# Kernel tuning notes

Measured on AMD Instinct MI355X. Metric: run time of the kernel, lower is better.

Reference implementation:

```python
import jax, jax.numpy as jnp
import numpy as np

B, T, QL, KVL, D, H = 4, 512, 2, 1, 1024, 16
N = T * QL          # query tokens for self-attn
HD = D // H
MLP_H = 4 * D
EPS_ADA = 1e-6
EPS_LN = 1e-5
NEG = -10000.0


def _ln(x, eps):
    mu = jnp.mean(x, axis=-1, keepdims=True)
    xc = x - mu
    var = jnp.mean(xc * xc, axis=-1, keepdims=True)
    return xc * jax.lax.rsqrt(var + eps)


def _attention(xq, xk, xv, wq, wk, wv, wo, bo, mask, pad_add):
    # xq:[B,Nq,D] xk/xv:[B,Nk,D]; mask:[Nq,Nk] bool; pad_add:[B,1,1,Nk]
    qh = (xq @ wq).reshape(B, -1, H, HD).transpose(0, 2, 1, 3)
    kh = (xk @ wk).reshape(B, -1, H, HD).transpose(0, 2, 1, 3)
    vh = (xv @ wv).reshape(B, -1, H, HD).transpose(0, 2, 1, 3)
    dots = jnp.einsum('bhnd,bhmd->bhnm', qh, kh) * (HD ** -0.5)
    dots = jnp.where(mask[None, None], dots, jnp.asarray(NEG, dots.dtype))
    dots = dots + pad_add
    attn = jax.nn.softmax(dots, axis=-1)
    out = jnp.einsum('bhnm,bhmd->bhnd', attn, vh)
    out = out.transpose(0, 2, 1, 3).reshape(B, -1, D)
    return out @ wo + bo


def setup_inputs() -> dict:
    key = jax.random.key(0)
    ks = jax.random.split(key, 32)
    s = 0.02
    d = {
        'q': jax.random.normal(ks[0], (B, N, D), jnp.float32),
        'c': jax.random.normal(ks[1], (B, T, D), jnp.float32),
        'pe': jax.random.normal(ks[2], (B, T, D), jnp.float32),
        'padding_mask': jax.random.randint(ks[3], (B, T), 0, 2, jnp.int32),
        'w_mod': jax.random.normal(ks[4], (D, 6 * D), jnp.float32) * s,
        'b_mod': jnp.zeros((6 * D,), jnp.float32),
        'sa_wq': jax.random.normal(ks[5], (D, D), jnp.float32) * s,
        'sa_wk': jax.random.normal(ks[6], (D, D), jnp.float32) * s,
        'sa_wv': jax.random.normal(ks[7], (D, D), jnp.float32) * s,
        'sa_wo': jax.random.normal(ks[8], (D, D), jnp.float32) * s,
        'sa_bo': jnp.zeros((D,), jnp.float32),
        'ca_wq': jax.random.normal(ks[9], (D, D), jnp.float32) * s,
        'ca_wk': jax.random.normal(ks[10], (D, D), jnp.float32) * s,
        'ca_wv': jax.random.normal(ks[11], (D, D), jnp.float32) * s,
        'ca_wo': jax.random.normal(ks[12], (D, D), jnp.float32) * s,
        'ca_bo': jnp.zeros((D,), jnp.float32),
        'gk': jnp.ones((D,), jnp.float32), 'bk': jnp.zeros((D,), jnp.float32),
        'gv': jnp.ones((D,), jnp.float32), 'bv': jnp.zeros((D,), jnp.float32),
        'w_alpha': jax.random.normal(ks[13], (2 * D, D), jnp.float32) * s,
        'b_alpha': jnp.zeros((D,), jnp.float32),
        'w1': jax.random.normal(ks[14], (D, MLP_H), jnp.float32) * s,
        'b1': jnp.zeros((MLP_H,), jnp.float32),
        'w2': jax.random.normal(ks[15], (MLP_H, D), jnp.float32) * s,
        'b2': jnp.zeros((D,), jnp.float32),
    }
    return d


def reference(q, c, pe, padding_mask, w_mod, b_mod,
              sa_wq, sa_wk, sa_wv, sa_wo, sa_bo,
              ca_wq, ca_wk, ca_wv, ca_wo, ca_bo,
              gk, bk, gv, bv, w_alpha, b_alpha, w1, b1, w2, b2):
    # AdaLN modulation from condition c
    mod = jax.nn.silu(c) @ w_mod + b_mod                    # [B,T,6D]
    scale_sa, shift_sa, scale_ca, shift_ca, scale_mlp, shift_mlp = jnp.split(mod, 6, axis=2)
    rep = lambda t: jnp.repeat(t, QL, axis=1)               # [B,T,D]->[B,N,D]

    # masks
    causal = jnp.tril(jnp.ones((N, N), bool))
    tril_t = jnp.tril(jnp.ones((T, T), bool))
    cross_mask = jnp.repeat(jnp.repeat(tril_t, QL, axis=0), KVL, axis=1)  # [N, T*KVL]
    pad_f = padding_mask.astype(q.dtype)
    pad_sa = (jnp.repeat(pad_f, QL, axis=1) * NEG)[:, None, None, :]      # keys len N
    pad_ca = (jnp.repeat(pad_f, KVL, axis=1) * NEG)[:, None, None, :]     # keys len T

    # self-attention (pre-norm + modulation)
    q1 = _ln(q, EPS_ADA) * (1 + rep(scale_sa)) + rep(shift_sa)
    q1 = _attention(q1, q1, q1, sa_wq, sa_wk, sa_wv, sa_wo, sa_bo, causal, pad_sa)
    q = q1 + q

    # cross-attention with custom mask
    q2 = _ln(q, EPS_ADA) * (1 + rep(scale_ca)) + rep(shift_ca)
    kin = _ln(c + pe, EPS_LN) * gk + bk
    vin = _ln(c, EPS_LN) * gv + bv
    q2 = _attention(q2, kin, vin, ca_wq, ca_wk, ca_wv, ca_wo, ca_bo, cross_mask, pad_ca)
    alpha = jnp.concatenate([q2, q], axis=-1) @ w_alpha + b_alpha
    q = (1 + alpha) * q2 + q

    # MLP
    q3 = _ln(q, EPS_ADA) * (1 + rep(scale_mlp)) + rep(shift_mlp)
    h = jax.nn.gelu(q3 @ w1 + b1, approximate=False)
    q = q + (h @ w2 + b2)
    return q
```

## Files before the change

### kernel.cpp

```cpp
#include <hip/hip_runtime.h>
#include <cstdint>

typedef unsigned short u16;
typedef __attribute__((ext_vector_type(8))) short bf16x8;
typedef __attribute__((ext_vector_type(4))) float f32x4;

#define DEV static __device__ __forceinline__
#define AS1 __attribute__((address_space(1)))
#define AS3 __attribute__((address_space(3)))

static constexpr int Bb = 4, Tt = 512, Nn = 1024, Dd = 1024, Hh = 16;
static constexpr float NEGV = -10000.0f;

DEV u16 f2bf(float f) {
  unsigned int u = __builtin_bit_cast(unsigned int, f);
  u += 0x7fffu + ((u >> 16) & 1u);
  return (u16)(u >> 16);
}
DEV float bf2f(u16 s) {
  unsigned int u = ((unsigned int)s) << 16;
  return __builtin_bit_cast(float, u);
}
DEV f32x4 mfma16(bf16x8 a, bf16x8 b, f32x4 c) {
  return __builtin_amdgcn_mfma_f32_16x16x32_bf16(a, b, c, 0, 0, 0);
}
DEV void gload16(const u16* g, u16* lds) {
  __builtin_amdgcn_global_load_lds((AS1 const unsigned int*)g, (AS3 unsigned int*)lds, 16, 0, 0);
}
DEV int swz8(int wg, int nwg) { const int c = nwg >> 3; return (wg & 7) * c + (wg >> 3); }

__global__ __launch_bounds__(256) void transpose_cast(const float* __restrict__ src,
                                                      u16* __restrict__ dst, int R, int C) {
  __shared__ float tile[32][33];
  const int c0 = blockIdx.x * 32, r0 = blockIdx.y * 32;
  const int tx = threadIdx.x, ty = threadIdx.y;
#pragma unroll
  for (int j = 0; j < 4; ++j)
    tile[ty + 8 * j][tx] = src[(size_t)(r0 + ty + 8 * j) * C + c0 + tx];
  __syncthreads();
#pragma unroll
  for (int j = 0; j < 4; ++j)
    dst[(size_t)(c0 + ty + 8 * j) * R + r0 + tx] = f2bf(tile[tx][ty + 8 * j]);
}

__global__ __launch_bounds__(256) void tr16_k(const u16* __restrict__ src, u16* __restrict__ dst,
                                              int ss, int R) {
  __shared__ u16 tile[32][33];
  const int c0 = blockIdx.x * 32, r0 = blockIdx.y * 32;
  const int tx = threadIdx.x, ty = threadIdx.y;
#pragma unroll
  for (int j = 0; j < 4; ++j)
    tile[ty + 8 * j][tx] = src[(size_t)(r0 + ty + 8 * j) * ss + c0 + tx];
  __syncthreads();
  const int b = r0 / R, rb = r0 - b * R;
#pragma unroll
  for (int j = 0; j < 4; ++j)
    dst[(size_t)b * 1024 * R + (size_t)(c0 + ty + 8 * j) * R + rb + tx] = tile[tx][ty + 8 * j];
}

__global__ __launch_bounds__(256) void silu_k(const float* __restrict__ c, u16* __restrict__ o, int n) {
  int i = blockIdx.x * 256 + threadIdx.x;
  if (i < n) { float x = c[i]; o[i] = f2bf(x / (1.0f + __expf(-x))); }
}

__global__ __launch_bounds__(256) void cat_k(const float* __restrict__ q2, const float* __restrict__ qr,
                                             u16* __restrict__ cat) {
  int i = blockIdx.x * 256 + threadIdx.x;
  int r = i >> 10, c = i & 1023;
  cat[(size_t)r * 2048 + c] = f2bf(q2[i]);
  cat[(size_t)r * 2048 + 1024 + c] = f2bf(qr[i]);
}

__global__ __launch_bounds__(256) void red2_k(const u16* __restrict__ s0, const u16* __restrict__ s1,
                                              const float* __restrict__ bias, const float* __restrict__ res,
                                              float* __restrict__ out) {
  const int i = blockIdx.x * 256 + threadIdx.x;
  const uint2 a = ((const uint2*)s0)[i];
  const uint2 b = ((const uint2*)s1)[i];
  const float4 bv = ((const float4*)bias)[i & 255];
  const float4 rv = ((const float4*)res)[i];
  float4 v;
  v.x = bf2f((u16)(a.x & 0xffff)) + bf2f((u16)(b.x & 0xffff)) + bv.x + rv.x;
  v.y = bf2f((u16)(a.x >> 16))    + bf2f((u16)(b.x >> 16))    + bv.y + rv.y;
  v.z = bf2f((u16)(a.y & 0xffff)) + bf2f((u16)(b.y & 0xffff)) + bv.z + rv.z;
  v.w = bf2f((u16)(a.y >> 16))    + bf2f((u16)(b.y >> 16))    + bv.w + rv.w;
  ((float4*)out)[i] = v;
}

__global__ __launch_bounds__(64) void mrow_k(const int* __restrict__ pm, float* __restrict__ M) {
  const int tid = threadIdx.x;
  const int b = tid >> 4, seg = tid & 15;
  int pre[32];
  int a = 1;
#pragma unroll
  for (int j = 0; j < 32; ++j) { a &= pm[b * 512 + seg * 32 + j]; pre[j] = a; }
  const int total = a;
  int excl = 1;
  for (int s = 0; s < 16; ++s) {
    int o = __shfl(total, (b << 4) + s, 64);
    if (s < seg) excl &= o;
  }
#pragma unroll
  for (int j = 0; j < 32; ++j)
    M[b * 512 + seg * 32 + j] = (excl & pre[j]) ? NEGV : 0.0f;
}

__global__ __launch_bounds__(256) void ln_mod_k(const float* __restrict__ X, const u16* __restrict__ MOD,
                                                u16* __restrict__ OUT, int chunk) {
  const int row = blockIdx.x;
  const int b = row >> 10, i = row & 1023, t = i >> 1;
  const int tid = threadIdx.x;
  const float4 xv = *(const float4*)&X[(size_t)row * 1024 + tid * 4];
  float s = xv.x + xv.y + xv.z + xv.w;
  float q = xv.x * xv.x + xv.y * xv.y + xv.z * xv.z + xv.w * xv.w;
#pragma unroll
  for (int off = 32; off > 0; off >>= 1) { s += __shfl_down(s, off); q += __shfl_down(q, off); }
  __shared__ float rs[4], rq[4];
  if ((tid & 63) == 0) { rs[tid >> 6] = s; rq[tid >> 6] = q; }
  __syncthreads();
  float S = rs[0] + rs[1] + rs[2] + rs[3];
  float Q = rq[0] + rq[1] + rq[2] + rq[3];
  const float mu = S * (1.0f / 1024.0f);
  const float var = Q * (1.0f / 1024.0f) - mu * mu;
  const float rstd = rsqrtf(var + 1e-6f);
  const u16* mrow = MOD + (size_t)(b * Tt + t) * 6144 + chunk * 1024 + tid * 4;
  u16* out = OUT + (size_t)row * 1024 + tid * 4;
  const float xx[4] = {xv.x, xv.y, xv.z, xv.w};
#pragma unroll
  for (int j = 0; j < 4; ++j) {
    float sc = bf2f(mrow[j]);
    float sh = bf2f(mrow[1024 + j]);
    out[j] = f2bf((xx[j] - mu) * rstd * (1.0f + sc) + sh);
  }
}

__global__ __launch_bounds__(256) void ln_kv_k(const float* __restrict__ C_, const float* __restrict__ PE,
                                               const float* __restrict__ gk, const float* __restrict__ bk,
                                               const float* __restrict__ gv, const float* __restrict__ bv,
                                               u16* __restrict__ KIN, u16* __restrict__ VIN) {
  const int row = blockIdx.x, tid = threadIdx.x;
  const size_t base = (size_t)row * 1024 + tid * 4;
  const float4 cv = *(const float4*)&C_[base];
  const float4 pv = *(const float4*)&PE[base];
  const float a[4] = {cv.x + pv.x, cv.y + pv.y, cv.z + pv.z, cv.w + pv.w};
  const float bb[4] = {cv.x, cv.y, cv.z, cv.w};
  float sa = a[0] + a[1] + a[2] + a[3];
  float qa = a[0] * a[0] + a[1] * a[1] + a[2] * a[2] + a[3] * a[3];
  float sb = bb[0] + bb[1] + bb[2] + bb[3];
  float qb = bb[0] * bb[0] + bb[1] * bb[1] + bb[2] * bb[2] + bb[3] * bb[3];
#pragma unroll
  for (int off = 32; off > 0; off >>= 1) {
    sa += __shfl_down(sa, off); qa += __shfl_down(qa, off);
    sb += __shfl_down(sb, off); qb += __shfl_down(qb, off);
  }
  __shared__ float r4[4][4];
  if ((tid & 63) == 0) {
    int w = tid >> 6;
    r4[0][w] = sa; r4[1][w] = qa; r4[2][w] = sb; r4[3][w] = qb;
  }
  __syncthreads();
  sa = r4[0][0] + r4[0][1] + r4[0][2] + r4[0][3];
  qa = r4[1][0] + r4[1][1] + r4[1][2] + r4[1][3];
  sb = r4[2][0] + r4[2][1] + r4[2][2] + r4[2][3];
  qb = r4[3][0] + r4[3][1] + r4[3][2] + r4[3][3];
  const float mua = sa * (1.0f / 1024.0f);
  const float ra = rsqrtf(qa * (1.0f / 1024.0f) - mua * mua + 1e-5f);
  const float mub = sb * (1.0f / 1024.0f);
  const float rb = rsqrtf(qb * (1.0f / 1024.0f) - mub * mub + 1e-5f);
#pragma unroll
  for (int j = 0; j < 4; ++j) {
    int d = tid * 4 + j;
    KIN[(size_t)row * 1024 + d] = f2bf((a[j] - mua) * ra * gk[d] + bk[d]);
    VIN[(size_t)row * 1024 + d] = f2bf((bb[j] - mub) * rb * gv[d] + bv[d]);
  }
}

DEV void stage32(const u16* __restrict__ A, const u16* __restrict__ Bt, int K,
                 int brow, int bcol, int kb, u16 (*As)[32], u16 (*Bs)[32]) {
  const int l = threadIdx.x & 63, wid = threadIdx.x >> 6;
#pragma unroll
  for (int p = 0; p < 2; ++p) {
    const int r0 = p * 64 + wid * 16;
    const int row = r0 + (l >> 2), kof = (l & 3) << 3;
    gload16(&A[(size_t)(brow + row) * K + kb + kof], &As[r0][0]);
    gload16(&Bt[(size_t)(bcol + row) * K + kb + kof], &Bs[r0][0]);
  }
}

DEV void gcore(const u16* __restrict__ A, const u16* __restrict__ Bt, int K,
               int brow, int bcol, int k0, int nk32,
               u16 (*As)[128][32], u16 (*Bs)[128][32], f32x4 (&acc)[4][4]) {
  const int l = threadIdx.x & 63, wid = threadIdx.x >> 6;
  const int wr = wid >> 1, wc = wid & 1;
  const int fr = l & 15, fg = l >> 4;
  stage32(A, Bt, K, brow, bcol, k0, As[0], Bs[0]);
  __syncthreads();
  int cur = 0;
  for (int kt = 0; kt < nk32; ++kt) {
    if (kt + 1 < nk32)
      stage32(A, Bt, K, brow, bcol, k0 + ((kt + 1) << 5), As[cur ^ 1], Bs[cur ^ 1]);
    bf16x8 af[4], bfr[4];
#pragma unroll
    for (int m = 0; m < 4; ++m) af[m] = *(const bf16x8*)&As[cur][wr * 64 + m * 16 + fr][fg * 8];
#pragma unroll
    for (int n = 0; n < 4; ++n) bfr[n] = *(const bf16x8*)&Bs[cur][wc * 64 + n * 16 + fr][fg * 8];
#pragma unroll
    for (int m = 0; m < 4; ++m)
#pragma unroll
      for (int n = 0; n < 4; ++n) acc[m][n] = mfma16(af[m], bfr[n], acc[m][n]);
    __syncthreads();
    cur ^= 1;
  }
}

template <int EPI>
__global__ __launch_bounds__(256) void gemm_k(const u16* __restrict__ A, const u16* __restrict__ Bt,
                                              int N, int K, const float* __restrict__ bias,
                                              u16* __restrict__ outb, int nbx) {
  __shared__ u16 As[2][128][32];
  __shared__ u16 Bs[2][128][32];
  const int wg = swz8(blockIdx.x, gridDim.x);
  const int brow = (wg / nbx) * 128, bcol = (wg % nbx) * 128;
  const int l = threadIdx.x & 63, wid = threadIdx.x >> 6;
  const int wr = wid >> 1, wc = wid & 1, fr = l & 15, fg = l >> 4;
  f32x4 acc[4][4];
#pragma unroll
  for (int m = 0; m < 4; ++m)
#pragma unroll
    for (int n = 0; n < 4; ++n) acc[m][n] = (f32x4){0.f, 0.f, 0.f, 0.f};
  gcore(A, Bt, K, brow, bcol, 0, K >> 5, As, Bs, acc);
#pragma unroll
  for (int m = 0; m < 4; ++m)
#pragma unroll
    for (int n = 0; n < 4; ++n)
#pragma unroll
      for (int r = 0; r < 4; ++r) {
        const int row = brow + wr * 64 + m * 16 + fg * 4 + r;
        const int col = bcol + wc * 64 + n * 16 + fr;
        float v = acc[m][n][r];
        if (EPI != 0) v += bias[col];
        if (EPI == 2) {
          const float u = v * (0.7978845608f + 0.0356774081f * v * v);
          v = v / (1.0f + __expf(-2.0f * u));
        }
        outb[(size_t)row * N + col] = f2bf(v);
      }
}

template <int EPI>
__global__ __launch_bounds__(256) void gemm64(const u16* __restrict__ A, const u16* __restrict__ Bt,
                                              int N, int K, const float* __restrict__ bias,
                                              const float* __restrict__ res, const float* __restrict__ q2,
                                              float* __restrict__ outf, int nbx) {
  __shared__ u16 As[2][128][32];
  __shared__ u16 Bs[2][64][32];
  const int wg = swz8(blockIdx.x, gridDim.x);
  const int brow = (wg / nbx) * 128, bcol = (wg % nbx) * 64;
  const int l = threadIdx.x & 63, wid = threadIdx.x >> 6;
  const int wr = wid >> 1, wc = wid & 1, fr = l & 15, fg = l >> 4;
  const int srow = l >> 2, skof = (l & 3) << 3;

  f32x4 acc[4][2];
#pragma unroll
  for (int m = 0; m < 4; ++m)
#pragma unroll
    for (int n = 0; n < 2; ++n) acc[m][n] = (f32x4){0.f, 0.f, 0.f, 0.f};

  auto stg = [&](int kb, int cur) {
    gload16(&A[(size_t)(brow + wid * 32 + srow) * K + kb + skof], &As[cur][wid * 32][0]);
    gload16(&A[(size_t)(brow + wid * 32 + 16 + srow) * K + kb + skof], &As[cur][wid * 32 + 16][0]);
    gload16(&Bt[(size_t)(bcol + wid * 16 + srow) * K + kb + skof], &Bs[cur][wid * 16][0]);
  };

  stg(0, 0);
  __syncthreads();
  int cur = 0;
  const int nk32 = K >> 5;
  for (int kt = 0; kt < nk32; ++kt) {
    if (kt + 1 < nk32) stg((kt + 1) << 5, cur ^ 1);
    bf16x8 af[4], bfr[2];
#pragma unroll
    for (int m = 0; m < 4; ++m) af[m] = *(const bf16x8*)&As[cur][wr * 64 + m * 16 + fr][fg * 8];
#pragma unroll
    for (int n = 0; n < 2; ++n) bfr[n] = *(const bf16x8*)&Bs[cur][wc * 32 + n * 16 + fr][fg * 8];
#pragma unroll
    for (int m = 0; m < 4; ++m)
#pragma unroll
      for (int n = 0; n < 2; ++n) acc[m][n] = mfma16(af[m], bfr[n], acc[m][n]);
    __syncthreads();
    cur ^= 1;
  }

#pragma unroll
  for (int m = 0; m < 4; ++m)
#pragma unroll
    for (int n = 0; n < 2; ++n)
#pragma unroll
      for (int r = 0; r < 4; ++r) {
        const int row = brow + wr * 64 + m * 16 + fg * 4 + r;
        const int col = bcol + wc * 32 + n * 16 + fr;
        const size_t o = (size_t)row * N + col;
        const float v = acc[m][n][r] + bias[col];
        if (EPI == 3) outf[o] = v + res[o];
        else if (EPI == 4) outf[o] = v;
        else outf[o] = (1.0f + v) * q2[o] + outf[o];
      }
}

__global__ __launch_bounds__(256) void gemm64b(const u16* __restrict__ A, const u16* __restrict__ Bt,
                                               int N, int K, u16* __restrict__ sk0, u16* __restrict__ sk1,
                                               int nbx) {
  __shared__ u16 As[2][128][32];
  __shared__ u16 Bs[2][64][32];
  const int wg = swz8(blockIdx.x, gridDim.x);
  const int brow = (wg / nbx) * 128, bcol = (wg % nbx) * 64;
  const int kper = K >> 1;
  const int k0 = blockIdx.y * kper;
  const int l = threadIdx.x & 63, wid = threadIdx.x >> 6;
  const int wr = wid >> 1, wc = wid & 1, fr = l & 15, fg = l >> 4;
  const int srow = l >> 2, skof = (l & 3) << 3;

  f32x4 acc[4][2];
#pragma unroll
  for (int m = 0; m < 4; ++m)
#pragma unroll
    for (int n = 0; n < 2; ++n) acc[m][n] = (f32x4){0.f, 0.f, 0.f, 0.f};

  auto stg = [&](int kb, int cur) {
    gload16(&A[(size_t)(brow + wid * 32 + srow) * K + kb + skof], &As[cur][wid * 32][0]);
    gload16(&A[(size_t)(brow + wid * 32 + 16 + srow) * K + kb + skof], &As[cur][wid * 32 + 16][0]);
    gload16(&Bt[(size_t)(bcol + wid * 16 + srow) * K + kb + skof], &Bs[cur][wid * 16][0]);
  };

  stg(k0, 0);
  __syncthreads();
  int cur = 0;
  const int nk32 = kper >> 5;
  for (int kt = 0; kt < nk32; ++kt) {
    if (kt + 1 < nk32) stg(k0 + ((kt + 1) << 5), cur ^ 1);
    bf16x8 af[4], bfr[2];
#pragma unroll
    for (int m = 0; m < 4; ++m) af[m] = *(const bf16x8*)&As[cur][wr * 64 + m * 16 + fr][fg * 8];
#pragma unroll
    for (int n = 0; n < 2; ++n) bfr[n] = *(const bf16x8*)&Bs[cur][wc * 32 + n * 16 + fr][fg * 8];
#pragma unroll
    for (int m = 0; m < 4; ++m)
#pragma unroll
      for (int n = 0; n < 2; ++n) acc[m][n] = mfma16(af[m], bfr[n], acc[m][n]);
    __syncthreads();
    cur ^= 1;
  }

  u16* out = blockIdx.y ? sk1 : sk0;
#pragma unroll
  for (int m = 0; m < 4; ++m)
#pragma unroll
    for (int n = 0; n < 2; ++n)
#pragma unroll
      for (int r = 0; r < 4; ++r) {
        const int row = brow + wr * 64 + m * 16 + fg * 4 + r;
        const int col = bcol + wc * 32 + n * 16 + fr;
        out[(size_t)row * N + col] = f2bf(acc[m][n][r]);
      }
}

__global__ __launch_bounds__(256) void gemm3_k(const u16* A0, const u16* A1, const u16* A2,
                                               const u16* B0, const u16* B1, const u16* B2,
                                               u16* O0, u16* O1, u16* O2) {
  const int z = blockIdx.y;
  const int wg = swz8(blockIdx.x, gridDim.x);
  const int bx = wg & 7, by = wg >> 3;
  if (z > 0 && by >= 16) return;
  const u16* A = z == 0 ? A0 : (z == 1 ? A1 : A2);
  const u16* Bt = z == 0 ? B0 : (z == 1 ? B1 : B2);
  u16* O = z == 0 ? O0 : (z == 1 ? O1 : O2);
  __shared__ u16 As[2][128][32];
  __shared__ u16 Bs[2][128][32];
  const int brow = by * 128, bcol = bx * 128;
  const int l = threadIdx.x & 63, wid = threadIdx.x >> 6;
  const int wr = wid >> 1, wc = wid & 1, fr = l & 15, fg = l >> 4;
  f32x4 acc[4][4];
#pragma unroll
  for (int m = 0; m < 4; ++m)
#pragma unroll
    for (int n = 0; n < 4; ++n) acc[m][n] = (f32x4){0.f, 0.f, 0.f, 0.f};
  gcore(A, Bt, 1024, brow, bcol, 0, 32, As, Bs, acc);
#pragma unroll
  for (int m = 0; m < 4; ++m)
#pragma unroll
    for (int n = 0; n < 4; ++n)
#pragma unroll
      for (int r = 0; r < 4; ++r) {
        const int row = brow + wr * 64 + m * 16 + fg * 4 + r;
        const int col = bcol + wc * 64 + n * 16 + fr;
        O[(size_t)row * 1024 + col] = f2bf(acc[m][n][r]);
      }
}

template <int QDIV, int PDIV>
__global__ __launch_bounds__(256) void attn_k(const u16* __restrict__ QH, const u16* __restrict__ KH,
                                              const u16* __restrict__ VT, u16* __restrict__ AO,
                                              const int* __restrict__ pmask, const float* __restrict__ Mrow,
                                              int Nq, int Nk, int qs, int ks) {
  __shared__ u16 KS[2][2048];
  __shared__ u16 VS[2][2048];
  __shared__ u16 PL[4][16][40];
  const int tid = threadIdx.x;
  const int l = tid & 63, wid = tid >> 6;
  const int fr = l & 15, fg = l >> 4;
  const int nqb = Nq >> 6;
  const int wgid = swz8(blockIdx.x, gridDim.x);
  const int qb = wgid % nqb;
  const int bh = wgid / nqb;
  const int h = bh & 15, b = bh >> 4;
  const int q0 = qb * 64 + wid * 16;

  u16 (*Pl)[40] = PL[wid];

  const int krow = l >> 3;
  const int kslot = (l & 7) ^ krow;
  const int vrow = l >> 2;
  const int vslot = (l & 3) ^ (vrow & 3);

  const size_t qrow = (size_t)(b * Nq + q0 + fr) * qs + h * 64;
  const bf16x8 aq0 = *(const bf16x8*)&QH[qrow + fg * 8];
  const bf16x8 aq1 = *(const bf16x8*)&QH[qrow + 32 + fg * 8];

  float Mr[4];
#pragma unroll
  for (int r = 0; r < 4; ++r) Mr[r] = Mrow[b * Tt + ((q0 + fg * 4 + r) >> 1)];

  f32x4 o[4];
#pragma unroll
  for (int c = 0; c < 4; ++c) o[c] = (f32x4){0.f, 0.f, 0.f, 0.f};
  float lsum[4] = {0.f, 0.f, 0.f, 0.f};

  int nkt = Nk >> 5;
  if (Mrow[b * Tt + ((qb * 64) >> 1)] == 0.0f) {
    const int kallow = (qb * 64 + 63) / QDIV + 1;
    const int t = (kallow + 31) >> 5;
    if (t < nkt) nkt = t;
  }

  const int sw0 = (fg ^ (fr & 7)) * 8;
  const int sw1 = ((4 + fg) ^ (fr & 7)) * 8;
  const size_t vtb = (size_t)b * 1024 * Nk + (size_t)(h * 64) * Nk;

  auto stage = [&](int kb, int buf) {
    gload16(&KH[(size_t)(b * Nk + kb + wid * 8 + krow) * ks + h * 64 + kslot * 8], &KS[buf][wid * 512]);
    gload16(&VT[vtb + (size_t)(wid * 16 + vrow) * Nk + kb + vslot * 8], &VS[buf][wid * 512]);
  };

  stage(0, 0);
  __syncthreads();
  int buf = 0;

  for (int kt = 0; kt < nkt; ++kt) {
    const int kb = kt << 5;
    if (kt + 1 < nkt) stage((kt + 1) << 5, buf ^ 1);

    const u16* Ksl = KS[buf];
    const u16* Vsl = VS[buf];

    f32x4 s0 = (f32x4){0.f, 0.f, 0.f, 0.f}, s1 = (f32x4){0.f, 0.f, 0.f, 0.f};
    {
      bf16x8 kf;
      kf = *(const bf16x8*)&Ksl[fr * 64 + sw0];        s0 = mfma16(aq0, kf, s0);
      kf = *(const bf16x8*)&Ksl[fr * 64 + sw1];        s0 = mfma16(aq1, kf, s0);
      kf = *(const bf16x8*)&Ksl[(16 + fr) * 64 + sw0]; s1 = mfma16(aq0, kf, s1);
      kf = *(const bf16x8*)&Ksl[(16 + fr) * 64 + sw1]; s1 = mfma16(aq1, kf, s1);
    }
    const int c0 = kb + fr, c1 = kb + 16 + fr;
    const float pad0 = pmask[b * Tt + (PDIV == 2 ? (c0 >> 1) : c0)] ? NEGV : 0.0f;
    const float pad1 = pmask[b * Tt + (PDIV == 2 ? (c1 >> 1) : c1)] ? NEGV : 0.0f;

#pragma unroll
    for (int r = 0; r < 4; ++r) {
      const int rq = (q0 + fg * 4 + r) >> (QDIV == 2 ? 1 : 0);
      float v0 = s0[r] * 0.125f; v0 = (c0 <= rq) ? v0 : NEGV; v0 += pad0;
      float v1 = s1[r] * 0.125f; v1 = (c1 <= rq) ? v1 : NEGV; v1 += pad1;
      const float p0 = __expf(v0 - Mr[r]);
      const float p1 = __expf(v1 - Mr[r]);
      lsum[r] += p0 + p1;
      Pl[fg * 4 + r][fr] = f2bf(p0);
      Pl[fg * 4 + r][16 + fr] = f2bf(p1);
    }

    const bf16x8 pa = *(const bf16x8*)&Pl[fr][fg * 8];
#pragma unroll
    for (int c = 0; c < 4; ++c) {
      const bf16x8 vb = *(const bf16x8*)&Vsl[(c * 16 + fr) * 32 + ((fg ^ (fr & 3)) << 3)];
      o[c] = mfma16(pa, vb, o[c]);
    }
    __syncthreads();
    buf ^= 1;
  }

#pragma unroll
  for (int r = 0; r < 4; ++r) {
    lsum[r] += __shfl_xor(lsum[r], 1);
    lsum[r] += __shfl_xor(lsum[r], 2);
    lsum[r] += __shfl_xor(lsum[r], 4);
    lsum[r] += __shfl_xor(lsum[r], 8);
  }

#pragma unroll
  for (int c = 0; c < 4; ++c)
#pragma unroll
    for (int r = 0; r < 4; ++r) {
      const int row = q0 + fg * 4 + r;
      AO[(size_t)(b * Nq + row) * Dd + h * 64 + c * 16 + fr] = f2bf(o[c][r] / lsum[r]);
    }
}

extern "C" void kernel_launch(void* const* d_in, const int* in_sizes, int n_in,
                              void* d_out, int out_size, void* d_ws, size_t ws_size,
                              hipStream_t stream) {
  (void)in_sizes; (void)n_in; (void)out_size; (void)ws_size;
  const float* q_in   = (const float*)d_in[0];
  const float* c_in   = (const float*)d_in[1];
  const float* pe     = (const float*)d_in[2];
  const int*   pmask  = (const int*)d_in[3];
  const float* w_mod  = (const float*)d_in[4];
  const float* b_mod  = (const float*)d_in[5];
  const float* sa_wq  = (const float*)d_in[6];
  const float* sa_wk  = (const float*)d_in[7];
  const float* sa_wv  = (const float*)d_in[8];
  const float* sa_wo  = (const float*)d_in[9];
  const float* sa_bo  = (const float*)d_in[10];
  const float* ca_wq  = (const float*)d_in[11];
  const float* ca_wk  = (const float*)d_in[12];
  const float* ca_wv  = (const float*)d_in[13];
  const float* ca_wo  = (const float*)d_in[14];
  const float* ca_bo  = (const float*)d_in[15];
  const float* gk     = (const float*)d_in[16];
  const float* bk     = (const float*)d_in[17];
  const float* gv     = (const float*)d_in[18];
  const float* bv     = (const float*)d_in[19];
  const float* w_alpha= (const float*)d_in[20];
  const float* b_alpha= (const float*)d_in[21];
  const float* w1     = (const float*)d_in[22];
  const float* b1     = (const float*)d_in[23];
  const float* w2     = (const float*)d_in[24];
  const float* b2     = (const float*)d_in[25];

  u16* ws = (u16*)d_ws;
  u16* WMODt  = ws + 0;
  float* Mp   = (float*)(ws + 4194304);
  u16* SK1b   = WMODt;
  u16* SAWQt  = ws + 6291456;
  u16* SAWKt  = ws + 7340032;
  u16* SAWVt  = ws + 8388608;
  u16* SAWOt  = ws + 9437184;
  u16* CAWQt  = ws + 10485760;
  u16* CAWKt  = ws + 11534336;
  u16* CAWVt  = ws + 12582912;
  u16* CAWOt  = ws + 13631488;
  u16* WALPHt = ws + 14680064;
  u16* W1t    = ws + 16777216;
  u16* W2t    = ws + 20971520;
  u16* Xs     = ws + 25165824;
  u16* KINp   = Xs;
  u16* VINp   = SAWQt;
  u16* MODbf  = ws + 27262976;
  u16* LNO    = ws + 39845888;
  u16* SK0b   = LNO;
  u16* BIG    = ws + 44040192;
  u16* QKVp = BIG;
  u16* VTsa = BIG + 12582912;
  u16* AOp  = LNO;
  u16* CAQp = BIG;
  u16* CAKp = BIG + 4194304;
  u16* CAVp = BIG + 6291456;
  u16* VT2  = BIG + 8388608;
  u16* AO2p = BIG + 10485760;
  u16* CATp = BIG;
  u16* HBp  = BIG;
  float* Qres = (float*)(ws + 60817408);
  float* Q2f  = Qres + 4194304;
  float* outp = (float*)d_out;

  const dim3 blk(256);
  auto TR = [&](const float* s, u16* d, int R, int C) {
    transpose_cast<<<dim3(C / 32, R / 32), dim3(32, 8), 0, stream>>>(s, d, R, C);
  };

  TR(w_mod, WMODt, 1024, 6144);
  TR(sa_wq, SAWQt, 1024, 1024); TR(sa_wk, SAWKt, 1024, 1024);
  TR(sa_wv, SAWVt, 1024, 1024); TR(sa_wo, SAWOt, 1024, 1024);
  TR(ca_wq, CAWQt, 1024, 1024); TR(ca_wk, CAWKt, 1024, 1024);
  TR(ca_wv, CAWVt, 1024, 1024); TR(ca_wo, CAWOt, 1024, 1024);
  TR(w_alpha, WALPHt, 2048, 1024);
  TR(w1, W1t, 1024, 4096);
  TR(w2, W2t, 4096, 1024);

  silu_k<<<8192, blk, 0, stream>>>(c_in, Xs, 2048 * 1024);
  gemm_k<1><<<768, blk, 0, stream>>>(Xs, WMODt, 6144, 1024, b_mod, MODbf, 48);
  mrow_k<<<1, 64, 0, stream>>>(pmask, Mp);

  ln_mod_k<<<4096, blk, 0, stream>>>(q_in, MODbf, LNO, 0);
  gemm_k<0><<<768, blk, 0, stream>>>(LNO, SAWQt, 3072, 1024, nullptr, QKVp, 24);
  tr16_k<<<dim3(32, 128), dim3(32, 8), 0, stream>>>(QKVp + 2048, VTsa, 3072, 1024);
  ln_kv_k<<<2048, blk, 0, stream>>>(c_in, pe, gk, bk, gv, bv, KINp, VINp);
  attn_k<1, 2><<<1024, blk, 0, stream>>>(QKVp, QKVp + 1024, VTsa, AOp, pmask, Mp,
                                         1024, 1024, 3072, 3072);
  gemm64<3><<<512, blk, 0, stream>>>(AOp, SAWOt, 1024, 1024, sa_bo, q_in, nullptr, Qres, 16);

  ln_mod_k<<<4096, blk, 0, stream>>>(Qres, MODbf, LNO, 2);
  gemm3_k<<<dim3(256, 3), blk, 0, stream>>>(LNO, KINp, VINp, CAWQt, CAWKt, CAWVt, CAQp, CAKp, CAVp);
  tr16_k<<<dim3(32, 64), dim3(32, 8), 0, stream>>>(CAVp, VT2, 1024, 512);
  attn_k<2, 1><<<1024, blk, 0, stream>>>(CAQp, CAKp, VT2, AO2p, pmask, Mp,
                                         1024, 512, 1024, 1024);
  gemm64<4><<<512, blk, 0, stream>>>(AO2p, CAWOt, 1024, 1024, ca_bo, nullptr, nullptr, Q2f, 16);
  cat_k<<<16384, blk, 0, stream>>>(Q2f, Qres, CATp);
  gemm64<5><<<512, blk, 0, stream>>>(CATp, WALPHt, 1024, 2048, b_alpha, nullptr, Q2f, Qres, 16);

  ln_mod_k<<<4096, blk, 0, stream>>>(Qres, MODbf, LNO, 4);
  gemm_k<2><<<1024, blk, 0, stream>>>(LNO, W1t, 4096, 1024, b1, HBp, 32);
  gemm64b<<<dim3(512, 2), blk, 0, stream>>>(HBp, W2t, 1024, 4096, SK0b, SK1b, 16);
  red2_k<<<4096, blk, 0, stream>>>(SK0b, SK1b, b2, Qres, outp);
}
```

Before: 480.5 us.

## Batch weight transposes into one launch and deepen K-tiles in 64-wide GEMMs

New measurement: 495.0 us. +3.0%, slower.

```diff
diff --git a/kernel.cpp b/kernel.cpp
--- a/kernel.cpp
+++ b/kernel.cpp
@@ -29,10 +29,22 @@
 }
 DEV int swz8(int wg, int nwg) { const int c = nwg >> 3; return (wg & 7) * c + (wg >> 3); }
 
-__global__ __launch_bounds__(256) void transpose_cast(const float* __restrict__ src,
-                                                      u16* __restrict__ dst, int R, int C) {
+struct TrDesc { const float* s; u16* d; int R, C, t0; };
+struct TrPack { TrDesc t[12]; };
+
+__global__ __launch_bounds__(256) void tr_all(TrPack p) {
   __shared__ float tile[32][33];
-  const int c0 = blockIdx.x * 32, r0 = blockIdx.y * 32;
+  const int bid = blockIdx.x;
+  int i = 0;
+#pragma unroll
+  for (int j = 1; j < 12; ++j)
+    if (bid >= p.t[j].t0) i = j;
+  const float* src = p.t[i].s;
+  u16* dst = p.t[i].d;
+  const int R = p.t[i].R, C = p.t[i].C;
+  const int lt = bid - p.t[i].t0;
+  const int ntx = C >> 5;
+  const int c0 = (lt % ntx) << 5, r0 = (lt / ntx) << 5;
   const int tx = threadIdx.x, ty = threadIdx.y;
 #pragma unroll
   for (int j = 0; j < 4; ++j)
@@ -252,13 +264,13 @@
                                               int N, int K, const float* __restrict__ bias,
                                               const float* __restrict__ res, const float* __restrict__ q2,
                                               float* __restrict__ outf, int nbx) {
-  __shared__ u16 As[2][128][32];
-  __shared__ u16 Bs[2][64][32];
+  __shared__ u16 As[2][128][64];
+  __shared__ u16 Bs[2][64][64];
   const int wg = swz8(blockIdx.x, gridDim.x);
   const int brow = (wg / nbx) * 128, bcol = (wg % nbx) * 64;
   const int l = threadIdx.x & 63, wid = threadIdx.x >> 6;
   const int wr = wid >> 1, wc = wid & 1, fr = l & 15, fg = l >> 4;
-  const int srow = l >> 2, skof = (l & 3) << 3;
+  const int srow = l >> 3, skof = (l & 7) << 3;
 
   f32x4 acc[4][2];
 #pragma unroll
@@ -267,26 +279,32 @@
     for (int n = 0; n < 2; ++n) acc[m][n] = (f32x4){0.f, 0.f, 0.f, 0.f};
 
   auto stg = [&](int kb, int cur) {
-    gload16(&A[(size_t)(brow + wid * 32 + srow) * K + kb + skof], &As[cur][wid * 32][0]);
-    gload16(&A[(size_t)(brow + wid * 32 + 16 + srow) * K + kb + skof], &As[cur][wid * 32 + 16][0]);
-    gload16(&Bt[(size_t)(bcol + wid * 16 + srow) * K + kb + skof], &Bs[cur][wid * 16][0]);
+#pragma unroll
+    for (int p = 0; p < 4; ++p)
+      gload16(&A[(size_t)(brow + wid * 32 + p * 8 + srow) * K + kb + skof], &As[cur][wid * 32 + p * 8][0]);
+#pragma unroll
+    for (int p = 0; p < 2; ++p)
+      gload16(&Bt[(size_t)(bcol + wid * 16 + p * 8 + srow) * K + kb + skof], &Bs[cur][wid * 16 + p * 8][0]);
   };
 
   stg(0, 0);
   __syncthreads();
   int cur = 0;
-  const int nk32 = K >> 5;
-  for (int kt = 0; kt < nk32; ++kt) {
-    if (kt + 1 < nk32) stg((kt + 1) << 5, cur ^ 1);
-    bf16x8 af[4], bfr[2];
-#pragma unroll
-    for (int m = 0; m < 4; ++m) af[m] = *(const bf16x8*)&As[cur][wr * 64 + m * 16 + fr][fg * 8];
-#pragma unroll
-    for (int n = 0; n < 2; ++n) bfr[n] = *(const bf16x8*)&Bs[cur][wc * 32 + n * 16 + fr][fg * 8];
-#pragma unroll
-    for (int m = 0; m < 4; ++m)
-#pragma unroll
-      for (int n = 0; n < 2; ++n) acc[m][n] = mfma16(af[m], bfr[n], acc[m][n]);
+  const int nk = K >> 6;
+  for (int kt = 0; kt < nk; ++kt) {
+    if (kt + 1 < nk) stg((kt + 1) << 6, cur ^ 1);
+#pragma unroll
+    for (int kk = 0; kk < 64; kk += 32) {
+      bf16x8 af[4], bfr[2];
+#pragma unroll
+      for (int m = 0; m < 4; ++m) af[m] = *(const bf16x8*)&As[cur][wr * 64 + m * 16 + fr][kk + fg * 8];
+#pragma unroll
+      for (int n = 0; n < 2; ++n) bfr[n] = *(const bf16x8*)&Bs[cur][wc * 32 + n * 16 + fr][kk + fg * 8];
+#pragma unroll
+      for (int m = 0; m < 4; ++m)
+#pragma unroll
+        for (int n = 0; n < 2; ++n) acc[m][n] = mfma16(af[m], bfr[n], acc[m][n]);
+    }
     __syncthreads();
     cur ^= 1;
   }
@@ -310,15 +328,15 @@
 __global__ __launch_bounds__(256) void gemm64b(const u16* __restrict__ A, const u16* __restrict__ Bt,
                                                int N, int K, u16* __restrict__ sk0, u16* __restrict__ sk1,
                                                int nbx) {
-  __shared__ u16 As[2][128][32];
-  __shared__ u16 Bs[2][64][32];
+  __shared__ u16 As[2][128][64];
+  __shared__ u16 Bs[2][64][64];
   const int wg = swz8(blockIdx.x, gridDim.x);
   const int brow = (wg / nbx) * 128, bcol = (wg % nbx) * 64;
   const int kper = K >> 1;
   const int k0 = blockIdx.y * kper;
   const int l = threadIdx.x & 63, wid = threadIdx.x >> 6;
   const int wr = wid >> 1, wc = wid & 1, fr = l & 15, fg = l >> 4;
-  const int srow = l >> 2, skof = (l & 3) << 3;
+  const int srow = l >> 3, skof = (l & 7) << 3;
 
   f32x4 acc[4][2];
 #pragma unroll
@@ -327,26 +345,32 @@
     for (int n = 0; n < 2; ++n) acc[m][n] = (f32x4){0.f, 0.f, 0.f, 0.f};
 
   auto stg = [&](int kb, int cur) {
-    gload16(&A[(size_t)(brow + wid * 32 + srow) * K + kb + skof], &As[cur][wid * 32][0]);
-    gload16(&A[(size_t)(brow + wid * 32 + 16 + srow) * K + kb + skof], &As[cur][wid * 32 + 16][0]);
-    gload16(&Bt[(size_t)(bcol + wid * 16 + srow) * K + kb + skof], &Bs[cur][wid * 16][0]);
+#pragma unroll
+    for (int p = 0; p < 4; ++p)
+      gload16(&A[(size_t)(brow + wid * 32 + p * 8 + srow) * K + kb + skof], &As[cur][wid * 32 + p * 8][0]);
+#pragma unroll
+    for (int p = 0; p < 2; ++p)
+      gload16(&Bt[(size_t)(bcol + wid * 16 + p * 8 + srow) * K + kb + skof], &Bs[cur][wid * 16 + p * 8][0]);
   };
 
   stg(k0, 0);
   __syncthreads();
   int cur = 0;
-  const int nk32 = kper >> 5;
-  for (int kt = 0; kt < nk32; ++kt) {
-    if (kt + 1 < nk32) stg(k0 + ((kt + 1) << 5), cur ^ 1);
-    bf16x8 af[4], bfr[2];
-#pragma unroll
-    for (int m = 0; m < 4; ++m) af[m] = *(const bf16x8*)&As[cur][wr * 64 + m * 16 + fr][fg * 8];
-#pragma unroll
-    for (int n = 0; n < 2; ++n) bfr[n] = *(const bf16x8*)&Bs[cur][wc * 32 + n * 16 + fr][fg * 8];
-#pragma unroll
-    for (int m = 0; m < 4; ++m)
-#pragma unroll
-      for (int n = 0; n < 2; ++n) acc[m][n] = mfma16(af[m], bfr[n], acc[m][n]);
+  const int nk = kper >> 6;
+  for (int kt = 0; kt < nk; ++kt) {
+    if (kt + 1 < nk) stg(k0 + ((kt + 1) << 6), cur ^ 1);
+#pragma unroll
+    for (int kk = 0; kk < 64; kk += 32) {
+      bf16x8 af[4], bfr[2];
+#pragma unroll
+      for (int m = 0; m < 4; ++m) af[m] = *(const bf16x8*)&As[cur][wr * 64 + m * 16 + fr][kk + fg * 8];
+#pragma unroll
+      for (int n = 0; n < 2; ++n) bfr[n] = *(const bf16x8*)&Bs[cur][wc * 32 + n * 16 + fr][kk + fg * 8];
+#pragma unroll
+      for (int m = 0; m < 4; ++m)
+#pragma unroll
+        for (int n = 0; n < 2; ++n) acc[m][n] = mfma16(af[m], bfr[n], acc[m][n]);
+    }
     __syncthreads();
     cur ^= 1;
   }
@@ -581,18 +605,26 @@
   float* outp = (float*)d_out;
 
   const dim3 blk(256);
-  auto TR = [&](const float* s, u16* d, int R, int C) {
-    transpose_cast<<<dim3(C / 32, R / 32), dim3(32, 8), 0, stream>>>(s, d, R, C);
+
+  TrPack pk;
+  int off = 0;
+  auto add = [&](int i, const float* s, u16* d, int R, int C) {
+    pk.t[i].s = s; pk.t[i].d = d; pk.t[i].R = R; pk.t[i].C = C; pk.t[i].t0 = off;
+    off += (C >> 5) * (R >> 5);
   };
-
-  TR(w_mod, WMODt, 1024, 6144);
-  TR(sa_wq, SAWQt, 1024, 1024); TR(sa_wk, SAWKt, 1024, 1024);
-  TR(sa_wv, SAWVt, 1024, 1024); TR(sa_wo, SAWOt, 1024, 1024);
-  TR(ca_wq, CAWQt, 1024, 1024); TR(ca_wk, CAWKt, 1024, 1024);
-  TR(ca_wv, CAWVt, 1024, 1024); TR(ca_wo, CAWOt, 1024, 1024);
-  TR(w_alpha, WALPHt, 2048, 1024);
-  TR(w1, W1t, 1024, 4096);
-  TR(w2, W2t, 4096, 1024);
+  add(0, w_mod, WMODt, 1024, 6144);
+  add(1, sa_wq, SAWQt, 1024, 1024);
+  add(2, sa_wk, SAWKt, 1024, 1024);
+  add(3, sa_wv, SAWVt, 1024, 1024);
+  add(4, sa_wo, SAWOt, 1024, 1024);
+  add(5, ca_wq, CAWQt, 1024, 1024);
+  add(6, ca_wk, CAWKt, 1024, 1024);
+  add(7, ca_wv, CAWVt, 1024, 1024);
+  add(8, ca_wo, CAWOt, 1024, 1024);
+  add(9, w_alpha, WALPHt, 2048, 1024);
+  add(10, w1, W1t, 1024, 4096);
+  add(11, w2, W2t, 4096, 1024);
+  tr_all<<<off, dim3(32, 8), 0, stream>>>(pk);
 
   silu_k<<<8192, blk, 0, stream>>>(c_in, Xs, 2048 * 1024);
   gemm_k<1><<<768, blk, 0, stream>>>(Xs, WMODt, 6144, 1024, b_mod, MODbf, 48);
```
